# Optimization experiments

Measured on AMD Instinct MI355X. Metric: run time of the kernel, lower is better.

## Reference

```python
import jax, jax.numpy as jnp
import numpy as np

B, L, LA, LL = 256, 512, 8, 64
V, D, P, HOPS = 100000, 300, 3, 3


def setup_inputs() -> dict:
    key = jax.random.key(0)
    ks = jax.random.split(key, 18)
    sc = 0.05
    return {
        "text":   jax.random.randint(ks[0], (B, L),  0, V),
        "aspect": jax.random.randint(ks[1], (B, LA), 0, V),
        "left":   jax.random.randint(ks[2], (B, LL), 0, V),
        # pretrained embedding table
        "embed": jax.random.normal(ks[3], (V, D), jnp.float32) * 0.1,
        # all Linear weights stored as [in, out] (y = x @ W + b)
        "Wx": jax.random.normal(ks[4], (D, D), jnp.float32) * sc,   # x_linear (no bias)
        "Ws": jax.random.normal(ks[5], (D, D), jnp.float32) * sc,   # s_linear (no bias)
        "Wk": jax.random.normal(ks[6], (D, D), jnp.float32) * sc,   # attention w_k
        "bk": jnp.zeros((D,), jnp.float32),
        "Wq": jax.random.normal(ks[7], (D, D), jnp.float32) * sc,   # attention w_q
        "bq": jnp.zeros((D,), jnp.float32),
        "w_mlp": jax.random.normal(ks[8], (2 * D,), jnp.float32) * sc,  # attention mlp score vector
        "Wproj": jax.random.normal(ks[9], (D, D), jnp.float32) * sc,    # attention proj
        "bproj": jnp.zeros((D,), jnp.float32),
        "Wm": jax.random.normal(ks[10], (D, D), jnp.float32) * sc,  # mlp
        "bm": jnp.zeros((D,), jnp.float32),
        "Wd": jax.random.normal(ks[11], (D, P), jnp.float32) * sc,  # dense
        "bd": jnp.zeros((P,), jnp.float32),
    }


def _forward(text, aspect, left, embed, Wx, Ws, Wk, bk, Wq, bq, w_mlp,
             Wproj, bproj, Wm, bm, Wd, bd):
    f32 = jnp.float32
    left_len = (left != 0).sum(-1)    # (B,)
    mem_len = (text != 0).sum(-1)     # (B,)
    asp_len = (aspect != 0).sum(-1)   # (B,)
    mem_len_f = mem_len.astype(f32)

    # aspect mean-pooled query (sum over all positions / nonzero count, as in torch code)
    asp_e = embed[aspect].sum(1) / asp_len.astype(f32)[:, None]   # (B, D)
    x = asp_e[:, None, :]                                         # (B, 1, D)

    memory = embed[text]                                          # (B, L, D)
    v_s = (memory.sum(1) / mem_len_f[:, None])[:, None, :]        # (B, 1, D)

    # SqueezeEmbedding (zero padding) + vectorized locationed_memory decay
    idx = jnp.arange(L, dtype=f32)[None, :]                       # (1, L)
    start = (left_len - asp_len).astype(f32)[:, None]             # aspect_start
    end = left_len.astype(f32)[:, None]                           # aspect_end
    l = jnp.where(idx < start, start - idx,
                  jnp.where(idx <= end, 0.0, idx - end))          # (B, L)
    w = 1.0 - l / mem_len_f[:, None]
    w = jnp.where(idx < mem_len_f[:, None], w, 0.0)               # zero padded positions
    memory = memory * w[:, :, None]                               # (B, L, D)

    for _ in range(HOPS):
        x = x @ Wx                                                # (B, 1, D)
        s = v_s @ Ws                                              # computed but unused (faithful)
        # Attention(score_function='mlp', n_head=1, hidden=D)
        kx = memory @ Wk + bk                                     # (B, L, D)
        qx = x @ Wq + bq                                          # (B, 1, D)
        # tanh(cat(kx, qx) @ w_mlp) == tanh(kx@w1 + qx@w2)
        score = jnp.tanh(kx @ w_mlp[:D] + qx @ w_mlp[D:])         # (B, L)
        score = jax.nn.softmax(score, axis=-1)
        v_ts = jnp.einsum('bl,bld->bd', score, kx)[:, None, :]    # (B, 1, D)
        v_ts = v_ts @ Wproj + bproj

    v_ns = (v_ts + v_s).reshape(text.shape[0], -1)                # (B, D)
    v_ms = jnp.tanh(v_ns @ Wm + bm)
    out = jax.nn.softmax(v_ms @ Wd + bd, axis=-1)                 # (B, P)
    return out


def reference(text, aspect, left, embed, Wx, Ws, Wk, bk, Wq, bq, w_mlp,
              Wproj, bproj, Wm, bm, Wd, bd):
    return _forward(text, aspect, left, embed, Wx, Ws, Wk, bk, Wq, bq,
                    w_mlp, Wproj, bproj, Wm, bm, Wd, bd)
```

## Files before the change

kernel.cpp:

```cpp
#include <hip/hip_runtime.h>
#include <math.h>

#define WS_KV   0
#define WS_C0   300
#define WS_C1   301
#define WS_G    304
#define WS_ACC  4096
#define WS_VSP  311296
#define WS_SCAL 618496

__device__ __forceinline__ float wred(float v) {
#pragma unroll
    for (int off = 32; off > 0; off >>= 1) v += __shfl_xor(v, off);
    return v;
}

__global__ __launch_bounds__(1024) void k_const(
    const float* __restrict__ Wx, const float* __restrict__ Wk,
    const float* __restrict__ bk, const float* __restrict__ Wq,
    const float* __restrict__ bq, const float* __restrict__ wmlp,
    float* __restrict__ ws)
{
    const int t = threadIdx.x, wv = t >> 6, lane = t & 63;
    __shared__ float uS[300], u2S[300], hA[300], hB[300];
    if (t < 300) { uS[t] = wmlp[t]; u2S[t] = wmlp[300 + t]; }
    __syncthreads();

    for (int j = wv; j < 300; j += 16) {
        float pk = 0.f, pq = 0.f;
#pragma unroll
        for (int m = 0; m < 5; ++m) {
            int idx = lane + 64 * m;
            if (idx < 300) {
                pk += Wk[j * 300 + idx] * uS[idx];
                pq += Wq[j * 300 + idx] * u2S[idx];
            }
        }
        pk = wred(pk); pq = wred(pq);
        if (lane == 0) { ws[WS_KV + j] = pk; hA[j] = pq; }
    }
    if (wv == 0) {
        float p = 0.f;
#pragma unroll
        for (int m = 0; m < 5; ++m) { int idx = lane + 64 * m; if (idx < 300) p += bk[idx] * uS[idx]; }
        p = wred(p);
        if (lane == 0) ws[WS_C0] = p;
    }
    if (wv == 1) {
        float p = 0.f;
#pragma unroll
        for (int m = 0; m < 5; ++m) { int idx = lane + 64 * m; if (idx < 300) p += bq[idx] * u2S[idx]; }
        p = wred(p);
        if (lane == 0) ws[WS_C1] = p;
    }
    __syncthreads();

#pragma unroll
    for (int hop = 0; hop < 3; ++hop) {
        const float* src = (hop & 1) ? hB : hA;
        float* dst = (hop & 1) ? hA : hB;
        for (int j = wv; j < 300; j += 16) {
            float p = 0.f;
#pragma unroll
            for (int m = 0; m < 5; ++m) {
                int idx = lane + 64 * m;
                if (idx < 300) p += Wx[j * 300 + idx] * src[idx];
            }
            p = wred(p);
            if (lane == 0) dst[j] = p;
        }
        __syncthreads();
    }
    if (t < 300) ws[WS_G + t] = hB[t];
}

__global__ __launch_bounds__(512, 6) void k_main(
    const int* __restrict__ text, const int* __restrict__ aspect,
    const int* __restrict__ left, const float* __restrict__ embed,
    float* __restrict__ ws)
{
    const int bid = blockIdx.x;
    const int b = bid >> 2, quarter = bid & 3;
    const int t = threadIdx.x, wv = t >> 6, lane = t & 63;

    __shared__ int   toksS[128];
    __shared__ int   atoksS[8];
    __shared__ __align__(16) float accW[8 * 300];
    __shared__ __align__(16) float vsW[8 * 300];
    __shared__ float denomW[8], qpart[5], sc[4];
    __shared__ int   cnts[3];

    if (t < 3) cnts[t] = 0;
    __syncthreads();

    const int tk = text[b * 512 + t];
    const bool predm = (tk != 0);
    if ((t >> 7) == quarter) toksS[t & 127] = tk;
    const bool predl = (t < 64) && (left[b * 64 + t] != 0);
    bool preda = false;
    if (t >= 64 && t < 72) {
        int ak = aspect[b * 8 + (t - 64)];
        atoksS[t - 64] = ak;
        preda = (ak != 0);
    }
    {
        unsigned long long m;
        m = __ballot(predm); if (lane == 0 && m) atomicAdd(&cnts[0], __popcll(m));
        m = __ballot(predl); if (lane == 0 && m) atomicAdd(&cnts[1], __popcll(m));
        m = __ballot(preda); if (lane == 0 && m) atomicAdd(&cnts[2], __popcll(m));
    }
    __syncthreads();

    if (wv < 5) {
        float val = 0.f;
        if (t < 300) {
            float s = 0.f;
#pragma unroll
            for (int a = 0; a < 8; ++a) s += embed[(size_t)atoksS[a] * 300 + t];
            val = s * ws[WS_G + t];
        }
        val = wred(val);
        if (lane == 0) qpart[wv] = val;
    }
    __syncthreads();
    if (t == 0) {
        float q = (qpart[0] + qpart[1] + qpart[2] + qpart[3] + qpart[4]) / (float)cnts[2];
        sc[0] = (float)cnts[0];
        sc[1] = (float)(cnts[1] - cnts[2]);
        sc[2] = (float)cnts[1];
        sc[3] = q + ws[WS_C0] + ws[WS_C1];
    }
    __syncthreads();
    const float mem_len_f = sc[0], startf = sc[1], endf = sc[2], qb = sc[3];

    const float4* kv4  = (const float4*)(ws + WS_KV);
    const float4* emb4 = (const float4*)embed;
    const bool hasB = (lane < 11);
    const float4 kva = kv4[lane];
    const float4 kvb = hasB ? kv4[64 + lane] : make_float4(0.f, 0.f, 0.f, 0.f);

    float4 accA = make_float4(0.f,0.f,0.f,0.f), accB = make_float4(0.f,0.f,0.f,0.f);
    float4 vsA  = make_float4(0.f,0.f,0.f,0.f), vsB  = make_float4(0.f,0.f,0.f,0.f);
    float denom = 0.f;
    const float posbase = (float)(quarter * 128);

    for (int it = 0; it < 8; ++it) {
        const int l0 = wv * 16 + 2 * it, l1 = l0 + 1;
        const int r0 = toksS[l0] * 75, r1 = toksS[l1] * 75;
        float4 a0 = emb4[r0 + lane];
        float4 a1 = emb4[r1 + lane];
        float4 b0 = hasB ? emb4[r0 + 64 + lane] : make_float4(0.f,0.f,0.f,0.f);
        float4 b1 = hasB ? emb4[r1 + 64 + lane] : make_float4(0.f,0.f,0.f,0.f);

        float pd0 = a0.x*kva.x + a0.y*kva.y + a0.z*kva.z + a0.w*kva.w
                  + b0.x*kvb.x + b0.y*kvb.y + b0.z*kvb.z + b0.w*kvb.w;
        float pd1 = a1.x*kva.x + a1.y*kva.y + a1.z*kva.z + a1.w*kva.w
                  + b1.x*kvb.x + b1.y*kvb.y + b1.z*kvb.z + b1.w*kvb.w;
#pragma unroll
        for (int off = 32; off > 0; off >>= 1) {
            pd0 += __shfl_xor(pd0, off);
            pd1 += __shfl_xor(pd1, off);
        }

        const float f0 = posbase + (float)l0, f1 = f0 + 1.f;
        float lv0 = (f0 < startf) ? (startf - f0) : ((f0 <= endf) ? 0.f : (f0 - endf));
        float lv1 = (f1 < startf) ? (startf - f1) : ((f1 <= endf) ? 0.f : (f1 - endf));
        float w0 = 1.f - lv0 / mem_len_f; w0 = (f0 < mem_len_f) ? w0 : 0.f;
        float w1 = 1.f - lv1 / mem_len_f; w1 = (f1 < mem_len_f) ? w1 : 0.f;

        const float p0 = expf(tanhf(w0 * pd0 + qb));
        const float p1 = expf(tanhf(w1 * pd1 + qb));
        const float pw0 = p0 * w0, pw1 = p1 * w1;

        accA.x += pw0*a0.x + pw1*a1.x;  accA.y += pw0*a0.y + pw1*a1.y;
        accA.z += pw0*a0.z + pw1*a1.z;  accA.w += pw0*a0.w + pw1*a1.w;
        accB.x += pw0*b0.x + pw1*b1.x;  accB.y += pw0*b0.y + pw1*b1.y;
        accB.z += pw0*b0.z + pw1*b1.z;  accB.w += pw0*b0.w + pw1*b1.w;
        vsA.x += a0.x + a1.x;  vsA.y += a0.y + a1.y;
        vsA.z += a0.z + a1.z;  vsA.w += a0.w + a1.w;
        vsB.x += b0.x + b1.x;  vsB.y += b0.y + b1.y;
        vsB.z += b0.z + b1.z;  vsB.w += b0.w + b1.w;
        denom += p0 + p1;
    }

    *(float4*)&accW[wv * 300 + 4 * lane] = accA;
    *(float4*)&vsW [wv * 300 + 4 * lane] = vsA;
    if (hasB) {
        *(float4*)&accW[wv * 300 + 256 + 4 * lane] = accB;
        *(float4*)&vsW [wv * 300 + 256 + 4 * lane] = vsB;
    }
    if (lane == 0) denomW[wv] = denom;
    __syncthreads();

    if (t < 300) {
        float ds = 0.f;
#pragma unroll
        for (int w = 0; w < 8; ++w) ds += denomW[w];
        float ms = 0.f, vs = 0.f;
#pragma unroll
        for (int w = 0; w < 8; ++w) { ms += accW[w * 300 + t]; vs += vsW[w * 300 + t]; }
        ws[WS_ACC + bid * 300 + t] = ms;
        ws[WS_VSP + bid * 300 + t] = vs;
        if (t == 0) { ws[WS_SCAL + bid * 2] = ds; ws[WS_SCAL + bid * 2 + 1] = mem_len_f; }
    }
}

__global__ __launch_bounds__(960) void k_tail(
    const float* __restrict__ Wk, const float* __restrict__ bk,
    const float* __restrict__ Wproj, const float* __restrict__ bproj,
    const float* __restrict__ Wm, const float* __restrict__ bm,
    const float* __restrict__ Wd, const float* __restrict__ bd,
    float* __restrict__ out, const float* __restrict__ ws)
{
    const int t = threadIdx.x;
    const int b = blockIdx.x;
    const int seg = t / 320, j = t - seg * 320;

    __shared__ float A[300], T[300], VSs[300], part[900], vms[300], lg[3];

    if (t < 300) {
        const int p0 = (b * 4) * 300 + t;
        float a = ws[WS_ACC + p0] + ws[WS_ACC + p0 + 300]
                + ws[WS_ACC + p0 + 600] + ws[WS_ACC + p0 + 900];
        float v = ws[WS_VSP + p0] + ws[WS_VSP + p0 + 300]
                + ws[WS_VSP + p0 + 600] + ws[WS_VSP + p0 + 900];
        const int s0 = b * 8;
        float d  = ws[WS_SCAL + s0] + ws[WS_SCAL + s0 + 2]
                 + ws[WS_SCAL + s0 + 4] + ws[WS_SCAL + s0 + 6];
        float ml = ws[WS_SCAL + s0 + 1];
        A[t]   = a / d;
        VSs[t] = v / ml;
    }
    __syncthreads();

    if (j < 300) {
        const int k0 = seg * 100;
        float acc = 0.f;
#pragma unroll 10
        for (int i = 0; i < 100; ++i) acc += A[k0 + i] * Wk[(k0 + i) * 300 + j];
        part[seg * 300 + j] = acc;
    }
    __syncthreads();
    if (t < 300) T[t] = part[t] + part[300 + t] + part[600 + t] + bk[t];
    __syncthreads();

    if (j < 300) {
        const int k0 = seg * 100;
        float acc = 0.f;
#pragma unroll 10
        for (int i = 0; i < 100; ++i) acc += T[k0 + i] * Wproj[(k0 + i) * 300 + j];
        part[seg * 300 + j] = acc;
    }
    __syncthreads();
    if (t < 300) A[t] = part[t] + part[300 + t] + part[600 + t] + bproj[t] + VSs[t];
    __syncthreads();

    if (j < 300) {
        const int k0 = seg * 100;
        float acc = 0.f;
#pragma unroll 10
        for (int i = 0; i < 100; ++i) acc += A[k0 + i] * Wm[(k0 + i) * 300 + j];
        part[seg * 300 + j] = acc;
    }
    __syncthreads();
    if (t < 300) vms[t] = tanhf(part[t] + part[300 + t] + part[600 + t] + bm[t]);
    __syncthreads();

    const int wv = t >> 6, lane = t & 63;
    if (wv < 3) {
        float p = 0.f;
#pragma unroll
        for (int k = 0; k < 5; ++k) { int d = lane + 64 * k; if (d < 300) p += vms[d] * Wd[d * 3 + wv]; }
        p = wred(p);
        if (lane == 0) lg[wv] = p + bd[wv];
    }
    __syncthreads();
    if (t == 0) {
        float l0 = lg[0], l1 = lg[1], l2 = lg[2];
        float mx = fmaxf(l0, fmaxf(l1, l2));
        float e0 = expf(l0 - mx), e1 = expf(l1 - mx), e2 = expf(l2 - mx);
        float s = e0 + e1 + e2;
        out[b * 3 + 0] = e0 / s;
        out[b * 3 + 1] = e1 / s;
        out[b * 3 + 2] = e2 / s;
    }
}

extern "C" void kernel_launch(void* const* d_in, const int* in_sizes, int n_in,
                              void* d_out, int out_size, void* d_ws, size_t ws_size,
                              hipStream_t stream)
{
    (void)in_sizes; (void)n_in; (void)out_size; (void)ws_size;
    const int*   text   = (const int*)d_in[0];
    const int*   aspect = (const int*)d_in[1];
    const int*   left   = (const int*)d_in[2];
    const float* embed  = (const float*)d_in[3];
    const float* Wx     = (const float*)d_in[4];
    const float* Wk     = (const float*)d_in[6];
    const float* bk     = (const float*)d_in[7];
    const float* Wq     = (const float*)d_in[8];
    const float* bq     = (const float*)d_in[9];
    const float* wmlp   = (const float*)d_in[10];
    const float* Wproj  = (const float*)d_in[11];
    const float* bproj  = (const float*)d_in[12];
    const float* Wm     = (const float*)d_in[13];
    const float* bm     = (const float*)d_in[14];
    const float* Wd     = (const float*)d_in[15];
    const float* bd     = (const float*)d_in[16];
    float* out = (float*)d_out;
    float* ws  = (float*)d_ws;

    hipLaunchKernelGGL(k_const, dim3(1), dim3(1024), 0, stream,
                       Wx, Wk, bk, Wq, bq, wmlp, ws);
    hipLaunchKernelGGL(k_main, dim3(1024), dim3(512), 0, stream,
                       text, aspect, left, embed, ws);
    hipLaunchKernelGGL(k_tail, dim3(256), dim3(960), 0, stream,
                       Wk, bk, Wproj, bproj, Wm, bm, Wd, bd, out, ws);
}
```

Baseline: 303.2 us.

## Split constant precompute across many blocks and hoist per-row stats into separate kernel

The single-block constant kernel is split into a 302-block prep kernel plus three 300-block hop kernels, so the Wx chain runs across many CUs instead of serially in one block. Per-row counts and the aspect query score move into a new k_row kernel, which removes the duplicated full-text scan and aspect gather from each of the four k_main blocks per row. k_main now processes four tokens per iteration to expose more memory-level parallelism, and uses fast exp-based tanh and __expf, with occupancy bounds lowered to 4. The trade-off is four extra kernel launches and slightly lower precision in the transcendental functions.

```diff
diff --git a/kernel.cpp b/kernel.cpp
--- a/kernel.cpp
+++ b/kernel.cpp
@@ -4,7 +4,9 @@
 #define WS_KV   0
 #define WS_C0   300
 #define WS_C1   301
-#define WS_G    304
+#define WS_H0   304
+#define WS_H1   640
+#define WS_ROW  2048
 #define WS_ACC  4096
 #define WS_VSP  311296
 #define WS_SCAL 618496
@@ -15,172 +17,187 @@
     return v;
 }
 
-__global__ __launch_bounds__(1024) void k_const(
-    const float* __restrict__ Wx, const float* __restrict__ Wk,
-    const float* __restrict__ bk, const float* __restrict__ Wq,
-    const float* __restrict__ bq, const float* __restrict__ wmlp,
-    float* __restrict__ ws)
-{
-    const int t = threadIdx.x, wv = t >> 6, lane = t & 63;
-    __shared__ float uS[300], u2S[300], hA[300], hB[300];
-    if (t < 300) { uS[t] = wmlp[t]; u2S[t] = wmlp[300 + t]; }
-    __syncthreads();
-
-    for (int j = wv; j < 300; j += 16) {
+__device__ __forceinline__ float ftanh(float z) {
+    float t = __expf(2.f * z);
+    return (t - 1.f) / (t + 1.f);
+}
+
+__global__ __launch_bounds__(64) void k_prep(
+    const float* __restrict__ Wk, const float* __restrict__ bk,
+    const float* __restrict__ Wq, const float* __restrict__ bq,
+    const float* __restrict__ wmlp, float* __restrict__ ws)
+{
+    const int lane = threadIdx.x;
+    const int j = blockIdx.x;
+    const float* u  = wmlp;
+    const float* u2 = wmlp + 300;
+    if (j < 300) {
         float pk = 0.f, pq = 0.f;
 #pragma unroll
         for (int m = 0; m < 5; ++m) {
             int idx = lane + 64 * m;
             if (idx < 300) {
-                pk += Wk[j * 300 + idx] * uS[idx];
-                pq += Wq[j * 300 + idx] * u2S[idx];
+                pk += Wk[j * 300 + idx] * u[idx];
+                pq += Wq[j * 300 + idx] * u2[idx];
             }
         }
         pk = wred(pk); pq = wred(pq);
-        if (lane == 0) { ws[WS_KV + j] = pk; hA[j] = pq; }
-    }
-    if (wv == 0) {
+        if (lane == 0) { ws[WS_KV + j] = pk; ws[WS_H0 + j] = pq; }
+    } else if (j == 300) {
         float p = 0.f;
 #pragma unroll
-        for (int m = 0; m < 5; ++m) { int idx = lane + 64 * m; if (idx < 300) p += bk[idx] * uS[idx]; }
+        for (int m = 0; m < 5; ++m) { int idx = lane + 64 * m; if (idx < 300) p += bk[idx] * u[idx]; }
         p = wred(p);
         if (lane == 0) ws[WS_C0] = p;
-    }
-    if (wv == 1) {
+    } else {
         float p = 0.f;
 #pragma unroll
-        for (int m = 0; m < 5; ++m) { int idx = lane + 64 * m; if (idx < 300) p += bq[idx] * u2S[idx]; }
+        for (int m = 0; m < 5; ++m) { int idx = lane + 64 * m; if (idx < 300) p += bq[idx] * u2[idx]; }
         p = wred(p);
         if (lane == 0) ws[WS_C1] = p;
     }
-    __syncthreads();
-
-#pragma unroll
-    for (int hop = 0; hop < 3; ++hop) {
-        const float* src = (hop & 1) ? hB : hA;
-        float* dst = (hop & 1) ? hA : hB;
-        for (int j = wv; j < 300; j += 16) {
-            float p = 0.f;
-#pragma unroll
-            for (int m = 0; m < 5; ++m) {
-                int idx = lane + 64 * m;
-                if (idx < 300) p += Wx[j * 300 + idx] * src[idx];
-            }
-            p = wred(p);
-            if (lane == 0) dst[j] = p;
-        }
-        __syncthreads();
-    }
-    if (t < 300) ws[WS_G + t] = hB[t];
-}
-
-__global__ __launch_bounds__(512, 6) void k_main(
+}
+
+__global__ __launch_bounds__(64) void k_hop(
+    const float* __restrict__ Wx, const float* __restrict__ src,
+    float* __restrict__ dst)
+{
+    const int lane = threadIdx.x;
+    const int j = blockIdx.x;
+    float p = 0.f;
+#pragma unroll
+    for (int m = 0; m < 5; ++m) {
+        int idx = lane + 64 * m;
+        if (idx < 300) p += Wx[j * 300 + idx] * src[idx];
+    }
+    p = wred(p);
+    if (lane == 0) dst[j] = p;
+}
+
+__global__ __launch_bounds__(512) void k_row(
     const int* __restrict__ text, const int* __restrict__ aspect,
     const int* __restrict__ left, const float* __restrict__ embed,
     float* __restrict__ ws)
 {
+    const int b = blockIdx.x;
+    const int t = threadIdx.x, wv = t >> 6, lane = t & 63;
+
+    __shared__ int   atoks[8];
+    __shared__ int   cntW[8];
+    __shared__ float qp[5];
+    __shared__ int   lCnt, aCnt;
+
+    const int tk = text[b * 512 + t];
+    {
+        unsigned long long m = __ballot(tk != 0);
+        if (lane == 0) cntW[wv] = __popcll(m);
+    }
+    if (wv == 0) {
+        unsigned long long m = __ballot(left[b * 64 + lane] != 0);
+        if (lane == 0) lCnt = __popcll(m);
+    }
+    if (wv == 1) {
+        int ak = (lane < 8) ? aspect[b * 8 + lane] : 0;
+        if (lane < 8) atoks[lane] = ak;
+        unsigned long long m = __ballot(lane < 8 && ak != 0);
+        if (lane == 0) aCnt = __popcll(m);
+    }
+    __syncthreads();
+
+    if (wv < 5) {
+        float v = 0.f;
+        if (t < 300) {
+            float s = 0.f;
+#pragma unroll
+            for (int a = 0; a < 8; ++a) s += embed[(size_t)atoks[a] * 300 + t];
+            v = s * ws[WS_H1 + t];
+        }
+        v = wred(v);
+        if (lane == 0) qp[wv] = v;
+    }
+    __syncthreads();
+
+    if (t == 0) {
+        int ml = 0;
+#pragma unroll
+        for (int w = 0; w < 8; ++w) ml += cntW[w];
+        float q = (qp[0] + qp[1] + qp[2] + qp[3] + qp[4]) / (float)aCnt
+                + ws[WS_C0] + ws[WS_C1];
+        ws[WS_ROW + b * 4 + 0] = (float)ml;
+        ws[WS_ROW + b * 4 + 1] = (float)(lCnt - aCnt);
+        ws[WS_ROW + b * 4 + 2] = (float)lCnt;
+        ws[WS_ROW + b * 4 + 3] = q;
+    }
+}
+
+__global__ __launch_bounds__(512, 4) void k_main(
+    const int* __restrict__ text, const float* __restrict__ embed,
+    float* __restrict__ ws)
+{
     const int bid = blockIdx.x;
     const int b = bid >> 2, quarter = bid & 3;
     const int t = threadIdx.x, wv = t >> 6, lane = t & 63;
 
     __shared__ int   toksS[128];
-    __shared__ int   atoksS[8];
     __shared__ __align__(16) float accW[8 * 300];
     __shared__ __align__(16) float vsW[8 * 300];
-    __shared__ float denomW[8], qpart[5], sc[4];
-    __shared__ int   cnts[3];
-
-    if (t < 3) cnts[t] = 0;
-    __syncthreads();
-
-    const int tk = text[b * 512 + t];
-    const bool predm = (tk != 0);
-    if ((t >> 7) == quarter) toksS[t & 127] = tk;
-    const bool predl = (t < 64) && (left[b * 64 + t] != 0);
-    bool preda = false;
-    if (t >= 64 && t < 72) {
-        int ak = aspect[b * 8 + (t - 64)];
-        atoksS[t - 64] = ak;
-        preda = (ak != 0);
-    }
-    {
-        unsigned long long m;
-        m = __ballot(predm); if (lane == 0 && m) atomicAdd(&cnts[0], __popcll(m));
-        m = __ballot(predl); if (lane == 0 && m) atomicAdd(&cnts[1], __popcll(m));
-        m = __ballot(preda); if (lane == 0 && m) atomicAdd(&cnts[2], __popcll(m));
-    }
-    __syncthreads();
-
-    if (wv < 5) {
-        float val = 0.f;
-        if (t < 300) {
-            float s = 0.f;
-#pragma unroll
-            for (int a = 0; a < 8; ++a) s += embed[(size_t)atoksS[a] * 300 + t];
-            val = s * ws[WS_G + t];
-        }
-        val = wred(val);
-        if (lane == 0) qpart[wv] = val;
-    }
-    __syncthreads();
-    if (t == 0) {
-        float q = (qpart[0] + qpart[1] + qpart[2] + qpart[3] + qpart[4]) / (float)cnts[2];
-        sc[0] = (float)cnts[0];
-        sc[1] = (float)(cnts[1] - cnts[2]);
-        sc[2] = (float)cnts[1];
-        sc[3] = q + ws[WS_C0] + ws[WS_C1];
-    }
+    __shared__ float denomW[8], sc[4];
+
+    if (t < 128) toksS[t] = text[b * 512 + quarter * 128 + t];
+    if (t >= 128 && t < 132) sc[t - 128] = ws[WS_ROW + b * 4 + (t - 128)];
     __syncthreads();
     const float mem_len_f = sc[0], startf = sc[1], endf = sc[2], qb = sc[3];
+    const float inv_ml = 1.f / mem_len_f;
 
     const float4* kv4  = (const float4*)(ws + WS_KV);
     const float4* emb4 = (const float4*)embed;
     const bool hasB = (lane < 11);
     const float4 kva = kv4[lane];
     const float4 kvb = hasB ? kv4[64 + lane] : make_float4(0.f, 0.f, 0.f, 0.f);
-
-    float4 accA = make_float4(0.f,0.f,0.f,0.f), accB = make_float4(0.f,0.f,0.f,0.f);
-    float4 vsA  = make_float4(0.f,0.f,0.f,0.f), vsB  = make_float4(0.f,0.f,0.f,0.f);
+    const float4 fz = make_float4(0.f, 0.f, 0.f, 0.f);
+
+    float4 accA = fz, accB = fz, vsA = fz, vsB = fz;
     float denom = 0.f;
     const float posbase = (float)(quarter * 128);
 
-    for (int it = 0; it < 8; ++it) {
-        const int l0 = wv * 16 + 2 * it, l1 = l0 + 1;
-        const int r0 = toksS[l0] * 75, r1 = toksS[l1] * 75;
-        float4 a0 = emb4[r0 + lane];
-        float4 a1 = emb4[r1 + lane];
-        float4 b0 = hasB ? emb4[r0 + 64 + lane] : make_float4(0.f,0.f,0.f,0.f);
-        float4 b1 = hasB ? emb4[r1 + 64 + lane] : make_float4(0.f,0.f,0.f,0.f);
-
-        float pd0 = a0.x*kva.x + a0.y*kva.y + a0.z*kva.z + a0.w*kva.w
-                  + b0.x*kvb.x + b0.y*kvb.y + b0.z*kvb.z + b0.w*kvb.w;
-        float pd1 = a1.x*kva.x + a1.y*kva.y + a1.z*kva.z + a1.w*kva.w
-                  + b1.x*kvb.x + b1.y*kvb.y + b1.z*kvb.z + b1.w*kvb.w;
+    for (int it = 0; it < 4; ++it) {
+        const int base = wv * 16 + 4 * it;
+        int rr[4];
+#pragma unroll
+        for (int k = 0; k < 4; ++k) rr[k] = toksS[base + k] * 75;
+        float4 A[4], Bv[4];
+#pragma unroll
+        for (int k = 0; k < 4; ++k) A[k] = emb4[rr[k] + lane];
+#pragma unroll
+        for (int k = 0; k < 4; ++k) Bv[k] = hasB ? emb4[rr[k] + 64 + lane] : fz;
+
+        float pd[4];
+#pragma unroll
+        for (int k = 0; k < 4; ++k)
+            pd[k] = A[k].x*kva.x + A[k].y*kva.y + A[k].z*kva.z + A[k].w*kva.w
+                  + Bv[k].x*kvb.x + Bv[k].y*kvb.y + Bv[k].z*kvb.z + Bv[k].w*kvb.w;
 #pragma unroll
         for (int off = 32; off > 0; off >>= 1) {
-            pd0 += __shfl_xor(pd0, off);
-            pd1 += __shfl_xor(pd1, off);
+#pragma unroll
+            for (int k = 0; k < 4; ++k) pd[k] += __shfl_xor(pd[k], off);
         }
 
-        const float f0 = posbase + (float)l0, f1 = f0 + 1.f;
-        float lv0 = (f0 < startf) ? (startf - f0) : ((f0 <= endf) ? 0.f : (f0 - endf));
-        float lv1 = (f1 < startf) ? (startf - f1) : ((f1 <= endf) ? 0.f : (f1 - endf));
-        float w0 = 1.f - lv0 / mem_len_f; w0 = (f0 < mem_len_f) ? w0 : 0.f;
-        float w1 = 1.f - lv1 / mem_len_f; w1 = (f1 < mem_len_f) ? w1 : 0.f;
-
-        const float p0 = expf(tanhf(w0 * pd0 + qb));
-        const float p1 = expf(tanhf(w1 * pd1 + qb));
-        const float pw0 = p0 * w0, pw1 = p1 * w1;
-
-        accA.x += pw0*a0.x + pw1*a1.x;  accA.y += pw0*a0.y + pw1*a1.y;
-        accA.z += pw0*a0.z + pw1*a1.z;  accA.w += pw0*a0.w + pw1*a1.w;
-        accB.x += pw0*b0.x + pw1*b1.x;  accB.y += pw0*b0.y + pw1*b1.y;
-        accB.z += pw0*b0.z + pw1*b1.z;  accB.w += pw0*b0.w + pw1*b1.w;
-        vsA.x += a0.x + a1.x;  vsA.y += a0.y + a1.y;
-        vsA.z += a0.z + a1.z;  vsA.w += a0.w + a1.w;
-        vsB.x += b0.x + b1.x;  vsB.y += b0.y + b1.y;
-        vsB.z += b0.z + b1.z;  vsB.w += b0.w + b1.w;
-        denom += p0 + p1;
+#pragma unroll
+        for (int k = 0; k < 4; ++k) {
+            const float f = posbase + (float)(base + k);
+            float lv = (f < startf) ? (startf - f) : ((f <= endf) ? 0.f : (f - endf));
+            float wgt = 1.f - lv * inv_ml;
+            wgt = (f < mem_len_f) ? wgt : 0.f;
+            const float p = __expf(ftanh(wgt * pd[k] + qb));
+            const float pw = p * wgt;
+            accA.x += pw * A[k].x;  accA.y += pw * A[k].y;
+            accA.z += pw * A[k].z;  accA.w += pw * A[k].w;
+            accB.x += pw * Bv[k].x; accB.y += pw * Bv[k].y;
+            accB.z += pw * Bv[k].z; accB.w += pw * Bv[k].w;
+            vsA.x += A[k].x;  vsA.y += A[k].y;  vsA.z += A[k].z;  vsA.w += A[k].w;
+            vsB.x += Bv[k].x; vsB.y += Bv[k].y; vsB.z += Bv[k].z; vsB.w += Bv[k].w;
+            denom += p;
+        }
     }
 
     *(float4*)&accW[wv * 300 + 4 * lane] = accA;
@@ -310,10 +327,12 @@
     float* out = (float*)d_out;
     float* ws  = (float*)d_ws;
 
-    hipLaunchKernelGGL(k_const, dim3(1), dim3(1024), 0, stream,
-                       Wx, Wk, bk, Wq, bq, wmlp, ws);
-    hipLaunchKernelGGL(k_main, dim3(1024), dim3(512), 0, stream,
-                       text, aspect, left, embed, ws);
+    hipLaunchKernelGGL(k_prep, dim3(302), dim3(64), 0, stream, Wk, bk, Wq, bq, wmlp, ws);
+    hipLaunchKernelGGL(k_hop, dim3(300), dim3(64), 0, stream, Wx, ws + WS_H0, ws + WS_H1);
+    hipLaunchKernelGGL(k_hop, dim3(300), dim3(64), 0, stream, Wx, ws + WS_H1, ws + WS_H0);
+    hipLaunchKernelGGL(k_hop, dim3(300), dim3(64), 0, stream, Wx, ws + WS_H0, ws + WS_H1);
+    hipLaunchKernelGGL(k_row, dim3(256), dim3(512), 0, stream, text, aspect, left, embed, ws);
+    hipLaunchKernelGGL(k_main, dim3(1024), dim3(512), 0, stream, text, embed, ws);
     hipLaunchKernelGGL(k_tail, dim3(256), dim3(960), 0, stream,
                        Wk, bk, Wproj, bproj, Wm, bm, Wd, bd, out, ws);
 }
```

Result: faster. 294.4 us (-2.9%).
